# Optimization experiments

Measured on AMD Instinct MI355X. Metric: run time of the kernel, lower is better.

The kernel has to match this reference:

```python
import jax, jax.numpy as jnp
import numpy as np

D_MODEL = 1024
D_STATE = 128
D_CONV = 4
EXPAND = 2
HEADDIM = 64
D_INNER = EXPAND * D_MODEL          # 2048
NHEADS = D_INNER // HEADDIM         # 32
NGROUPS = 1
CONV_DIM = D_INNER + 2 * NGROUPS * D_STATE            # 2304
D_IN_PROJ = 2 * D_INNER + 2 * NGROUPS * D_STATE + NHEADS  # 4384
NUM_CLASS = 48
BATCH = 2
SEQLEN = 512


def setup_inputs() -> dict:
    key = jax.random.key(0)
    ks = jax.random.split(key, 8)
    s = 0.02
    inputs = jax.random.normal(ks[0], (BATCH, SEQLEN, D_MODEL), jnp.float32)
    W_in = jax.random.normal(ks[1], (D_MODEL, D_IN_PROJ), jnp.float32) * s
    conv_w = jax.random.normal(ks[2], (CONV_DIM, D_CONV), jnp.float32) * 0.2
    conv_b = jnp.zeros((CONV_DIM,), jnp.float32)
    # dt_bias = inverse-softplus of dt sampled in [1e-3, 0.1] (mamba init)
    dt = jnp.exp(jax.random.uniform(ks[3], (NHEADS,), jnp.float32) * (np.log(0.1) - np.log(1e-3)) + np.log(1e-3))
    dt_bias = dt + jnp.log(-jnp.expm1(-dt))
    A_log = jnp.log(jax.random.uniform(ks[4], (NHEADS,), jnp.float32, 1.0, 16.0))
    D = jnp.ones((NHEADS,), jnp.float32)
    norm_w = jnp.ones((D_INNER,), jnp.float32)
    W_out = jax.random.normal(ks[5], (D_INNER, D_MODEL), jnp.float32) * s
    W_cls = jax.random.normal(ks[6], (D_INNER, NUM_CLASS), jnp.float32) * s
    b_cls = jnp.zeros((NUM_CLASS,), jnp.float32)
    return {"inputs": inputs, "W_in": W_in, "conv_w": conv_w, "conv_b": conv_b,
            "dt_bias": dt_bias, "A_log": A_log, "D": D, "norm_w": norm_w,
            "W_out": W_out, "W_cls": W_cls, "b_cls": b_cls}


def _forward(inputs, W_in, conv_w, conv_b, dt_bias, A_log, D, norm_w, W_out, W_cls, b_cls):
    B, L, _ = inputs.shape
    zxbcdt = inputs @ W_in                                     # (B,L,4384)
    z, xBC, dt = jnp.split(zxbcdt, [D_INNER, D_INNER + CONV_DIM], axis=-1)
    dt = jax.nn.softplus(dt + dt_bias)                         # (B,L,H)
    # causal depthwise conv over time on (x,B,C)
    xBC_t = jnp.pad(jnp.transpose(xBC, (0, 2, 1)), ((0, 0), (0, 0), (D_CONV - 1, 0)))
    xBC_c = jax.lax.conv_general_dilated(xBC_t, conv_w[:, None, :], (1,), 'VALID',
                                         feature_group_count=CONV_DIM)
    xBC = jax.nn.silu(jnp.transpose(xBC_c, (0, 2, 1)) + conv_b)
    x, Bm, Cm = jnp.split(xBC, [D_INNER, D_INNER + D_STATE], axis=-1)
    x = x.reshape(B, L, NHEADS, HEADDIM)
    A = -jnp.exp(A_log)                                        # (H,)
    dA = jnp.exp(dt * A)                                       # (B,L,H)

    def step(state, inp):
        # state: (B,H,P,N) -- selective SSM recurrence (chunk_size=1 path)
        x_t, B_t, C_t, dt_t, dA_t = inp
        state = state * dA_t[:, :, None, None] + jnp.einsum('bhp,bn,bh->bhpn', x_t, B_t, dt_t)
        y_t = jnp.einsum('bhpn,bn->bhp', state, C_t)
        return state, y_t

    state0 = jnp.zeros((B, NHEADS, HEADDIM, D_STATE), inputs.dtype)
    xs = (jnp.transpose(x, (1, 0, 2, 3)), jnp.transpose(Bm, (1, 0, 2)),
          jnp.transpose(Cm, (1, 0, 2)), jnp.transpose(dt, (1, 0, 2)),
          jnp.transpose(dA, (1, 0, 2)))
    _, ys = jax.lax.scan(step, state0, xs)                     # ys: (L,B,H,P)
    y = jnp.transpose(ys, (1, 0, 2, 3)) + D[None, None, :, None] * x
    y = y.reshape(B, L, D_INNER)
    # gated RMSNorm: rmsnorm(y * silu(z)) * weight
    y = y * jax.nn.silu(z)
    y = y * jax.lax.rsqrt(jnp.mean(y * y, axis=-1, keepdims=True) + 1e-5) * norm_w
    # hidden_states (d_inner=2048) go through the per-timestep classifier
    preds = y @ W_cls + b_cls                                  # (B,L,num_class)
    return preds


def reference(inputs, W_in, conv_w, conv_b, dt_bias, A_log, D, norm_w, W_out, W_cls, b_cls):
    return _forward(inputs, W_in, conv_w, conv_b, dt_bias, A_log, D, norm_w, W_out, W_cls, b_cls)
```

## Files before the change

kernel.cpp:

```cpp
#include <hip/hip_runtime.h>
#include <hip/hip_bf16.h>
#include <cstdint>

#define BATCH 2
#define SEQLEN 512
#define BL (BATCH*SEQLEN)
#define DMODEL 1024
#define DINNER 2048
#define NHEADS 32
#define HEADDIM 64
#define DSTATE 128
#define CONVDIM 2304
#define DINPROJ 4384
#define NPROJPAD 4480
#define NCLS 48
#define QC 64
#define NCH 8

typedef short bf16x8 __attribute__((ext_vector_type(8)));
typedef float f32x4  __attribute__((ext_vector_type(4)));
typedef unsigned int u32;
typedef const __attribute__((address_space(1))) u32 gu32;
typedef __attribute__((address_space(3))) u32 lu32;

static __device__ __forceinline__ void gl16(const void* g, void* l) {
    __builtin_amdgcn_global_load_lds((gu32*)g, (lu32*)l, 16, 0, 0);
}

static __device__ __forceinline__ unsigned short f2bf(float f) {
    unsigned u = __float_as_uint(f);
    unsigned r = (u + 0x7FFFu + ((u >> 16) & 1u)) >> 16;
    return (unsigned short)r;
}
static __device__ __forceinline__ float bf2f(unsigned short u) {
    return __uint_as_float(((unsigned)u) << 16);
}

__global__ __launch_bounds__(256) void k_cvt_a(const float* __restrict__ in,
                                               unsigned short* __restrict__ out) {
    int i = (blockIdx.x * 256 + threadIdx.x) * 4;
    float4 v = *(const float4*)(in + i);
    ushort4 o;
    o.x = f2bf(v.x); o.y = f2bf(v.y); o.z = f2bf(v.z); o.w = f2bf(v.w);
    *(ushort4*)(out + i) = o;
}

__global__ __launch_bounds__(256) void k_transpose_w(const float* __restrict__ W,
                                                     unsigned short* __restrict__ Wt) {
    __shared__ float tile[32][33];
    int n0 = blockIdx.x * 32;
    int k0 = blockIdx.y * 32;
    int tx = threadIdx.x & 31;
    int ty = threadIdx.x >> 5;
#pragma unroll
    for (int i = 0; i < 4; ++i) {
        int k = k0 + ty + i * 8;
        tile[ty + i * 8][tx] = W[(size_t)k * DINPROJ + n0 + tx];
    }
    __syncthreads();
#pragma unroll
    for (int i = 0; i < 4; ++i) {
        int n = n0 + ty + i * 8;
        Wt[(size_t)n * DMODEL + k0 + tx] = f2bf(tile[tx][ty + i * 8]);
    }
}

__global__ __launch_bounds__(256) void k_prep_cls(const float* __restrict__ W,
                                                  const float* __restrict__ bcls,
                                                  unsigned short* __restrict__ Wt,
                                                  float* __restrict__ out) {
    int bid = blockIdx.x;
    if (bid < 192) {
        int i = bid * 256 + threadIdx.x;
        out[i] = bcls[i % NCLS];
    } else {
        int n = bid - 192;
        for (int k = threadIdx.x; k < DINNER; k += 256)
            Wt[(size_t)n * DINNER + k] = f2bf(W[(size_t)k * NCLS + n]);
    }
}

__global__ __launch_bounds__(256) void k_gemm_in(const unsigned short* __restrict__ A,
                                                 const unsigned short* __restrict__ Bt,
                                                 unsigned short* __restrict__ C) {
    __shared__ unsigned short As[2 * 4096];
    __shared__ unsigned short Bs[2 * 4096];
    const int tid  = threadIdx.x;
    const int m0   = blockIdx.y * 128;
    const int n0   = blockIdx.x * 128;
    const int w    = tid >> 6;
    const int lane = tid & 63;
    const int wm   = w >> 1, wn = w & 1;
    const int fr   = lane & 15, fq = lane >> 4;
    const int srow = w * 16 + (lane >> 2);
    const int skg  = (lane & 3) * 8;
    const unsigned short* gA0 = A  + (size_t)(m0 + srow) * DMODEL + skg;
    const unsigned short* gA1 = gA0 + (size_t)64 * DMODEL;
    const unsigned short* gB0 = Bt + (size_t)(n0 + srow) * DMODEL + skg;
    const unsigned short* gB1 = gB0 + (size_t)64 * DMODEL;

    f32x4 acc[4][4] = {};
    for (int k0 = 0; k0 < DMODEL; k0 += 64) {
        __syncthreads();
#pragma unroll
        for (int hh = 0; hh < 2; ++hh) {
            int kg = k0 + hh * 32;
            gl16(gA0 + kg, As + hh * 4096 + w * 512);
            gl16(gA1 + kg, As + hh * 4096 + 2048 + w * 512);
            gl16(gB0 + kg, Bs + hh * 4096 + w * 512);
            gl16(gB1 + kg, Bs + hh * 4096 + 2048 + w * 512);
        }
        __syncthreads();
#pragma unroll
        for (int hh = 0; hh < 2; ++hh) {
            bf16x8 af[4], bf[4];
#pragma unroll
            for (int mt = 0; mt < 4; ++mt)
                af[mt] = *(const bf16x8*)(&As[hh * 4096 + (wm * 64 + mt * 16 + fr) * 32 + fq * 8]);
#pragma unroll
            for (int nt = 0; nt < 4; ++nt)
                bf[nt] = *(const bf16x8*)(&Bs[hh * 4096 + (wn * 64 + nt * 16 + fr) * 32 + fq * 8]);
#pragma unroll
            for (int mt = 0; mt < 4; ++mt)
#pragma unroll
                for (int nt = 0; nt < 4; ++nt)
                    acc[mt][nt] = __builtin_amdgcn_mfma_f32_16x16x32_bf16(af[mt], bf[nt], acc[mt][nt], 0, 0, 0);
        }
    }
#pragma unroll
    for (int mt = 0; mt < 4; ++mt) {
#pragma unroll
        for (int nt = 0; nt < 4; ++nt) {
            int col = n0 + wn * 64 + nt * 16 + fr;
            if (col < DINPROJ) {
#pragma unroll
                for (int r = 0; r < 4; ++r) {
                    int row = m0 + wm * 64 + mt * 16 + fq * 4 + r;
                    C[(size_t)row * DINPROJ + col] = f2bf(acc[mt][nt][r]);
                }
            }
        }
    }
}

__global__ __launch_bounds__(256) void k_conv_dt(const unsigned short* __restrict__ zx,
                                                 const float* __restrict__ conv_w,
                                                 const float* __restrict__ conv_b,
                                                 const float* __restrict__ dt_bias,
                                                 float* __restrict__ xbc,
                                                 float* __restrict__ dtb) {
    int row = blockIdx.y;
    int c   = blockIdx.x * 256 + threadIdx.x;
    int b = row >> 9, l = row & 511;
    if (c < CONVDIM) {
        float acc = conv_b[c];
#pragma unroll
        for (int j = 0; j < 4; ++j) {
            int ls = l - 3 + j;
            float v = (ls >= 0) ? bf2f(zx[((size_t)(b * SEQLEN + ls)) * DINPROJ + DINNER + c]) : 0.f;
            acc += v * conv_w[c * 4 + j];
        }
        float s = acc / (1.f + expf(-acc));
        xbc[(size_t)row * CONVDIM + c] = s;
    } else if (c < CONVDIM + NHEADS) {
        int h = c - CONVDIM;
        float raw = bf2f(zx[(size_t)row * DINPROJ + (DINNER + CONVDIM) + h]) + dt_bias[h];
        float dt = (raw > 20.f) ? raw : log1pf(expf(raw));
        dtb[row * NHEADS + h] = dt;
    }
}

__global__ __launch_bounds__(256) void k_chunk(const float* __restrict__ xbc,
                                               const float* __restrict__ dtb,
                                               const float* __restrict__ A_log,
                                               const float* __restrict__ Dvec,
                                               float* __restrict__ yb,
                                               float* __restrict__ Sc_g,
                                               float* __restrict__ lam_g,
                                               float* __restrict__ esc_g) {
    const int gid = blockIdx.x;
    const int c = gid & 7;
    const int h = (gid >> 3) & 31;
    const int b = gid >> 8;
    const int row0 = b * SEQLEN + c * QC;

    __shared__ float cumS[QC], wS[QC], dtS[QC];
    __shared__ unsigned short Xt[QC][72];
    __shared__ unsigned short Bs[QC][136];
    __shared__ unsigned short BtW[DSTATE][72];
    __shared__ unsigned short Cs[QC][136];
    __shared__ unsigned short Gs[QC][72];

    const int tid = threadIdx.x;
    if (tid < 64) {
        float dtv = dtb[(size_t)(row0 + tid) * NHEADS + h];
        float nA = -expf(A_log[h]);
        float x = dtv * nA;
#pragma unroll
        for (int off = 1; off < 64; off <<= 1) {
            float v = __shfl_up(x, off, 64);
            if (tid >= off) x += v;
        }
        float cumTot = __shfl(x, 63, 64);
        cumS[tid] = x;
        dtS[tid] = dtv;
        wS[tid] = expf(cumTot - x) * dtv;
        esc_g[(size_t)gid * QC + tid] = expf(x);
        if (tid == 0) lam_g[gid] = expf(cumTot);
    }
    __syncthreads();

    {
        int row = tid >> 2;
        int g = tid & 3;
        const float* rp = xbc + (size_t)(row0 + row) * CONVDIM;
        float wrow = wS[row];
#pragma unroll
        for (int i = 0; i < 4; ++i) {
            float4 v = *(const float4*)(rp + h * HEADDIM + g * 16 + i * 4);
            int p = g * 16 + i * 4;
            Xt[p + 0][row] = f2bf(v.x);
            Xt[p + 1][row] = f2bf(v.y);
            Xt[p + 2][row] = f2bf(v.z);
            Xt[p + 3][row] = f2bf(v.w);
        }
#pragma unroll
        for (int i = 0; i < 8; ++i) {
            int n = g * 32 + i * 4;
            float4 v = *(const float4*)(rp + DINNER + n);
            ushort4 u;
            u.x = f2bf(v.x); u.y = f2bf(v.y); u.z = f2bf(v.z); u.w = f2bf(v.w);
            *(ushort4*)(&Bs[row][n]) = u;
            BtW[n + 0][row] = f2bf(v.x * wrow);
            BtW[n + 1][row] = f2bf(v.y * wrow);
            BtW[n + 2][row] = f2bf(v.z * wrow);
            BtW[n + 3][row] = f2bf(v.w * wrow);
        }
#pragma unroll
        for (int i = 0; i < 8; ++i) {
            int n = g * 32 + i * 4;
            float4 v = *(const float4*)(rp + DINNER + DSTATE + n);
            ushort4 u;
            u.x = f2bf(v.x); u.y = f2bf(v.y); u.z = f2bf(v.z); u.w = f2bf(v.w);
            *(ushort4*)(&Cs[row][n]) = u;
        }
    }
    __syncthreads();

    const int w = tid >> 6, lane = tid & 63;
    const int fr = lane & 15, fq = lane >> 4, fk = (lane >> 4) * 8;

    f32x4 accG[4] = {};
#pragma unroll
    for (int kk = 0; kk < 4; ++kk) {
        bf16x8 a = *(const bf16x8*)(&Cs[w * 16 + fr][kk * 32 + fk]);
#pragma unroll
        for (int nt = 0; nt < 4; ++nt) {
            bf16x8 bb = *(const bf16x8*)(&Bs[nt * 16 + fr][kk * 32 + fk]);
            accG[nt] = __builtin_amdgcn_mfma_f32_16x16x32_bf16(a, bb, accG[nt], 0, 0, 0);
        }
    }
#pragma unroll
    for (int nt = 0; nt < 4; ++nt) {
        int s = nt * 16 + fr;
        float cs = cumS[s], dts = dtS[s];
#pragma unroll
        for (int r = 0; r < 4; ++r) {
            int t = w * 16 + fq * 4 + r;
            float val = (s <= t) ? accG[nt][r] * expf(cumS[t] - cs) * dts : 0.f;
            Gs[t][s] = f2bf(val);
        }
    }
    __syncthreads();

    f32x4 accY[4] = {};
#pragma unroll
    for (int kk = 0; kk < 2; ++kk) {
        bf16x8 a = *(const bf16x8*)(&Gs[w * 16 + fr][kk * 32 + fk]);
#pragma unroll
        for (int pt = 0; pt < 4; ++pt) {
            bf16x8 bb = *(const bf16x8*)(&Xt[pt * 16 + fr][kk * 32 + fk]);
            accY[pt] = __builtin_amdgcn_mfma_f32_16x16x32_bf16(a, bb, accY[pt], 0, 0, 0);
        }
    }
    f32x4 accS[8] = {};
#pragma unroll
    for (int kk = 0; kk < 2; ++kk) {
        bf16x8 a = *(const bf16x8*)(&Xt[w * 16 + fr][kk * 32 + fk]);
#pragma unroll
        for (int nt = 0; nt < 8; ++nt) {
            bf16x8 bb = *(const bf16x8*)(&BtW[nt * 16 + fr][kk * 32 + fk]);
            accS[nt] = __builtin_amdgcn_mfma_f32_16x16x32_bf16(a, bb, accS[nt], 0, 0, 0);
        }
    }
    float Dh = Dvec[h];
#pragma unroll
    for (int pt = 0; pt < 4; ++pt) {
        int p = pt * 16 + fr;
#pragma unroll
        for (int r = 0; r < 4; ++r) {
            int t = w * 16 + fq * 4 + r;
            float xv = xbc[(size_t)(row0 + t) * CONVDIM + h * HEADDIM + p];
            yb[(size_t)(row0 + t) * DINNER + h * HEADDIM + p] = accY[pt][r] + Dh * xv;
        }
    }
    float* scp = Sc_g + (size_t)gid * (HEADDIM * DSTATE);
#pragma unroll
    for (int nt = 0; nt < 8; ++nt) {
        int n = nt * 16 + fr;
#pragma unroll
        for (int r = 0; r < 4; ++r) {
            int p = w * 16 + fq * 4 + r;
            scp[p * DSTATE + n] = accS[nt][r];
        }
    }
}

__global__ __launch_bounds__(256) void k_chain(const float* __restrict__ Sc_g,
                                               const float* __restrict__ lam_g,
                                               unsigned short* __restrict__ Sin_bf) {
    int bh = blockIdx.x >> 2;
    int sl = blockIdx.x & 3;
    int tid = threadIdx.x;
    float s[8];
#pragma unroll
    for (int i = 0; i < 8; ++i) s[i] = 0.f;
    for (int c = 0; c < NCH; ++c) {
        size_t base = (size_t)(bh * NCH + c) * (HEADDIM * DSTATE) + sl * 2048 + tid * 8;
#pragma unroll
        for (int j = 0; j < 8; j += 4) {
            ushort4 u;
            u.x = f2bf(s[j + 0]); u.y = f2bf(s[j + 1]);
            u.z = f2bf(s[j + 2]); u.w = f2bf(s[j + 3]);
            *(ushort4*)(Sin_bf + base + j) = u;
        }
        float lam = lam_g[bh * NCH + c];
#pragma unroll
        for (int j = 0; j < 8; j += 4) {
            float4 v = *(const float4*)(Sc_g + base + j);
            s[j + 0] = s[j + 0] * lam + v.x;
            s[j + 1] = s[j + 1] * lam + v.y;
            s[j + 2] = s[j + 2] * lam + v.z;
            s[j + 3] = s[j + 3] * lam + v.w;
        }
    }
}

__global__ __launch_bounds__(256) void k_cross(const float* __restrict__ xbc,
                                               const float* __restrict__ esc_g,
                                               const unsigned short* __restrict__ Sin_bf,
                                               float* __restrict__ yb) {
    const int gid = blockIdx.x;
    const int c = gid & 7;
    const int h = (gid >> 3) & 31;
    const int b = gid >> 8;
    const int row0 = b * SEQLEN + c * QC;
    __shared__ unsigned short Ct[QC][136];
    __shared__ unsigned short Ss[QC][136];
    const int tid = threadIdx.x;
    {
        int row = tid >> 2, g = tid & 3;
        const float* rp = xbc + (size_t)(row0 + row) * CONVDIM + DINNER + DSTATE;
        float esc = esc_g[(size_t)gid * QC + row];
#pragma unroll
        for (int i = 0; i < 8; ++i) {
            int n = g * 32 + i * 4;
            float4 v = *(const float4*)(rp + n);
            ushort4 u;
            u.x = f2bf(v.x * esc); u.y = f2bf(v.y * esc);
            u.z = f2bf(v.z * esc); u.w = f2bf(v.w * esc);
            *(ushort4*)(&Ct[row][n]) = u;
        }
        const uint4* sp = (const uint4*)(Sin_bf + (size_t)gid * (HEADDIM * DSTATE));
#pragma unroll
        for (int i = 0; i < 4; ++i) {
            uint4 v = sp[row * 16 + g * 4 + i];
            *(uint4*)(&Ss[row][g * 32 + i * 8]) = v;
        }
    }
    __syncthreads();
    const int w = tid >> 6, lane = tid & 63;
    const int fr = lane & 15, fq = lane >> 4, fk = (lane >> 4) * 8;
    f32x4 acc[4] = {};
#pragma unroll
    for (int kk = 0; kk < 4; ++kk) {
        bf16x8 a = *(const bf16x8*)(&Ct[w * 16 + fr][kk * 32 + fk]);
#pragma unroll
        for (int pt = 0; pt < 4; ++pt) {
            bf16x8 bb = *(const bf16x8*)(&Ss[pt * 16 + fr][kk * 32 + fk]);
            acc[pt] = __builtin_amdgcn_mfma_f32_16x16x32_bf16(a, bb, acc[pt], 0, 0, 0);
        }
    }
#pragma unroll
    for (int pt = 0; pt < 4; ++pt) {
        int p = pt * 16 + fr;
#pragma unroll
        for (int r = 0; r < 4; ++r) {
            int t = w * 16 + fq * 4 + r;
            size_t yi = (size_t)(row0 + t) * DINNER + h * HEADDIM + p;
            yb[yi] += acc[pt][r];
        }
    }
}

__global__ __launch_bounds__(256) void k_gate_norm(const unsigned short* __restrict__ zx,
                                                   const float* __restrict__ nw,
                                                   const float* __restrict__ y,
                                                   unsigned short* __restrict__ Gbf) {
    int row = blockIdx.x;
    int tid = threadIdx.x;
    const unsigned short* zrow = zx + (size_t)row * DINPROJ;
    const float* yr = y + (size_t)row * DINNER;
    float g[8];
    float ss = 0.f;
#pragma unroll
    for (int i = 0; i < 2; ++i) {
        int c = tid * 4 + i * 1024;
        float4 yv = *(const float4*)(yr + c);
        ushort4 zv = *(const ushort4*)(zrow + c);
        float zs[4] = {bf2f(zv.x), bf2f(zv.y), bf2f(zv.z), bf2f(zv.w)};
        float ys[4] = {yv.x, yv.y, yv.z, yv.w};
#pragma unroll
        for (int k = 0; k < 4; ++k) {
            float sil = zs[k] / (1.f + expf(-zs[k]));
            float gg = ys[k] * sil;
            g[i * 4 + k] = gg;
            ss += gg * gg;
        }
    }
#pragma unroll
    for (int off = 32; off >= 1; off >>= 1) ss += __shfl_xor(ss, off, 64);
    __shared__ float wsum[4];
    if ((tid & 63) == 0) wsum[tid >> 6] = ss;
    __syncthreads();
    float tot = wsum[0] + wsum[1] + wsum[2] + wsum[3];
    float scale = rsqrtf(tot / (float)DINNER + 1e-5f);
#pragma unroll
    for (int i = 0; i < 2; ++i) {
        int c = tid * 4 + i * 1024;
        float4 nv = *(const float4*)(nw + c);
        ushort4 o;
        o.x = f2bf(g[i * 4 + 0] * scale * nv.x);
        o.y = f2bf(g[i * 4 + 1] * scale * nv.y);
        o.z = f2bf(g[i * 4 + 2] * scale * nv.z);
        o.w = f2bf(g[i * 4 + 3] * scale * nv.w);
        *(ushort4*)(Gbf + (size_t)row * DINNER + c) = o;
    }
}

__global__ __launch_bounds__(256) void k_cls_mfma(const unsigned short* __restrict__ G,
                                                  const unsigned short* __restrict__ Wt,
                                                  float* __restrict__ out) {
    __shared__ unsigned short Gs[64][72];
    __shared__ unsigned short Ws[48][72];
    const int m0  = blockIdx.x * 64;
    const int k00 = blockIdx.y * 256;
    const int tid = threadIdx.x;
    const int w = tid >> 6, lane = tid & 63;
    const int fr = lane & 15, fq = lane >> 4, fk = fq * 8;
    f32x4 acc[3] = {};
    for (int ks = 0; ks < 4; ++ks) {
        int k0 = k00 + ks * 64;
        __syncthreads();
        {
            int row = tid >> 2, seg = (tid & 3) * 16;
            const unsigned short* gp = G + (size_t)(m0 + row) * DINNER + k0 + seg;
            *(uint4*)(&Gs[row][seg])     = *(const uint4*)(gp);
            *(uint4*)(&Gs[row][seg + 8]) = *(const uint4*)(gp + 8);
        }
        if (tid < 192) {
            int row = tid >> 2, seg = (tid & 3) * 16;
            const unsigned short* wp = Wt + (size_t)row * DINNER + k0 + seg;
            *(uint4*)(&Ws[row][seg])     = *(const uint4*)(wp);
            *(uint4*)(&Ws[row][seg + 8]) = *(const uint4*)(wp + 8);
        }
        __syncthreads();
#pragma unroll
        for (int kk = 0; kk < 2; ++kk) {
            bf16x8 a = *(const bf16x8*)(&Gs[w * 16 + fr][kk * 32 + fk]);
#pragma unroll
            for (int nt = 0; nt < 3; ++nt) {
                bf16x8 bb = *(const bf16x8*)(&Ws[nt * 16 + fr][kk * 32 + fk]);
                acc[nt] = __builtin_amdgcn_mfma_f32_16x16x32_bf16(a, bb, acc[nt], 0, 0, 0);
            }
        }
    }
#pragma unroll
    for (int nt = 0; nt < 3; ++nt) {
        int col = nt * 16 + fr;
#pragma unroll
        for (int r = 0; r < 4; ++r) {
            int row = m0 + w * 16 + fq * 4 + r;
            atomicAdd(&out[(size_t)row * NCLS + col], acc[nt][r]);
        }
    }
}

extern "C" void kernel_launch(void* const* d_in, const int* in_sizes, int n_in,
                              void* d_out, int out_size, void* d_ws, size_t ws_size,
                              hipStream_t stream) {
    const float* inputs  = (const float*)d_in[0];
    const float* W_in    = (const float*)d_in[1];
    const float* conv_w  = (const float*)d_in[2];
    const float* conv_b  = (const float*)d_in[3];
    const float* dt_bias = (const float*)d_in[4];
    const float* A_log   = (const float*)d_in[5];
    const float* Dvec    = (const float*)d_in[6];
    const float* norm_w  = (const float*)d_in[7];
    const float* W_cls   = (const float*)d_in[9];
    const float* b_cls   = (const float*)d_in[10];
    float* out = (float*)d_out;

    float* ws   = (float*)d_ws;
    unsigned short* zxb = (unsigned short*)ws;
    float* xbc  = ws   + (size_t)BL * DINPROJ / 2 + 512;
    float* dtb  = xbc  + (size_t)BL * CONVDIM;
    float* yb   = dtb  + (size_t)BL * NHEADS;
    float* Sc_g = yb   + (size_t)BL * DINNER;
    float* lam_g= Sc_g + (size_t)BATCH * NHEADS * NCH * HEADDIM * DSTATE;
    float* esc_g= lam_g+ (size_t)BATCH * NHEADS * NCH;
    unsigned short* Sin_bf = (unsigned short*)(esc_g + (size_t)BATCH * NHEADS * NCH * QC);
    unsigned short* abf    = Sin_bf + (size_t)BATCH * NHEADS * NCH * HEADDIM * DSTATE;
    unsigned short* wtbf   = abf + (size_t)BL * DMODEL;
    unsigned short* wclsbf = wtbf + (size_t)NPROJPAD * DMODEL;
    unsigned short* Gbf    = (unsigned short*)Sc_g;

    k_cvt_a<<<dim3(BL * DMODEL / (256 * 4)), dim3(256), 0, stream>>>(inputs, abf);
    k_transpose_w<<<dim3(DINPROJ / 32, DMODEL / 32), dim3(256), 0, stream>>>(W_in, wtbf);
    k_prep_cls<<<dim3(240), dim3(256), 0, stream>>>(W_cls, b_cls, wclsbf, out);
    k_gemm_in<<<dim3(NPROJPAD / 128, BL / 128), dim3(256), 0, stream>>>(abf, wtbf, zxb);
    k_conv_dt<<<dim3(10, BL), dim3(256), 0, stream>>>(zxb, conv_w, conv_b, dt_bias, xbc, dtb);
    k_chunk<<<dim3(BATCH * NHEADS * NCH), dim3(256), 0, stream>>>(xbc, dtb, A_log, Dvec,
                                                                  yb, Sc_g, lam_g, esc_g);
    k_chain<<<dim3(BATCH * NHEADS * 4), dim3(256), 0, stream>>>(Sc_g, lam_g, Sin_bf);
    k_cross<<<dim3(BATCH * NHEADS * NCH), dim3(256), 0, stream>>>(xbc, esc_g, Sin_bf, yb);
    k_gate_norm<<<dim3(BL), dim3(256), 0, stream>>>(zxb, norm_w, yb, Gbf);
    k_cls_mfma<<<dim3(BL / 64, 8), dim3(256), 0, stream>>>(Gbf, wclsbf, out);
}
```

Measured before the change: 171.4 us.

## Fuse prep kernels, fold conv/dt into chunk kernels, halve GEMM N-tile, bf16 states

Merges the three preprocessing kernels into one launch and removes the separate conv+dt kernel. The causal conv, SiLU and softplus are now recomputed inside k_chunk and k_cross straight from the bf16 projection output, so the fp32 xbc/dtb intermediates are never written. The input GEMM tile shrinks from 128 to 64 columns to launch more blocks, and per-chunk states are stored in bf16 to halve chain-kernel traffic. In exchange, the C/B conv columns are recomputed redundantly across heads, the conv reads are strided by row, and chunk states lose precision.

```diff
diff --git a/kernel.cpp b/kernel.cpp
--- a/kernel.cpp
+++ b/kernel.cpp
@@ -36,47 +36,49 @@
     return __uint_as_float(((unsigned)u) << 16);
 }
 
-__global__ __launch_bounds__(256) void k_cvt_a(const float* __restrict__ in,
-                                               unsigned short* __restrict__ out) {
-    int i = (blockIdx.x * 256 + threadIdx.x) * 4;
-    float4 v = *(const float4*)(in + i);
-    ushort4 o;
-    o.x = f2bf(v.x); o.y = f2bf(v.y); o.z = f2bf(v.z); o.w = f2bf(v.w);
-    *(ushort4*)(out + i) = o;
-}
-
-__global__ __launch_bounds__(256) void k_transpose_w(const float* __restrict__ W,
-                                                     unsigned short* __restrict__ Wt) {
+__global__ __launch_bounds__(256) void k_prep(const float* __restrict__ in,
+                                              unsigned short* __restrict__ abf,
+                                              const float* __restrict__ W,
+                                              unsigned short* __restrict__ Wt,
+                                              const float* __restrict__ Wcls,
+                                              const float* __restrict__ bcls,
+                                              unsigned short* __restrict__ Wtc,
+                                              float* __restrict__ out) {
     __shared__ float tile[32][33];
-    int n0 = blockIdx.x * 32;
-    int k0 = blockIdx.y * 32;
-    int tx = threadIdx.x & 31;
-    int ty = threadIdx.x >> 5;
-#pragma unroll
-    for (int i = 0; i < 4; ++i) {
-        int k = k0 + ty + i * 8;
-        tile[ty + i * 8][tx] = W[(size_t)k * DINPROJ + n0 + tx];
-    }
-    __syncthreads();
-#pragma unroll
-    for (int i = 0; i < 4; ++i) {
-        int n = n0 + ty + i * 8;
-        Wt[(size_t)n * DMODEL + k0 + tx] = f2bf(tile[tx][ty + i * 8]);
-    }
-}
-
-__global__ __launch_bounds__(256) void k_prep_cls(const float* __restrict__ W,
-                                                  const float* __restrict__ bcls,
-                                                  unsigned short* __restrict__ Wt,
-                                                  float* __restrict__ out) {
     int bid = blockIdx.x;
-    if (bid < 192) {
-        int i = bid * 256 + threadIdx.x;
-        out[i] = bcls[i % NCLS];
+    int tid = threadIdx.x;
+    if (bid < 1024) {
+        int i = (bid * 256 + tid) * 4;
+        float4 v = *(const float4*)(in + i);
+        ushort4 o;
+        o.x = f2bf(v.x); o.y = f2bf(v.y); o.z = f2bf(v.z); o.w = f2bf(v.w);
+        *(ushort4*)(abf + i) = o;
+    } else if (bid < 1024 + 4384) {
+        int t = bid - 1024;
+        int n0 = (t % 137) * 32;
+        int k0 = (t / 137) * 32;
+        int tx = tid & 31, ty = tid >> 5;
+#pragma unroll
+        for (int i = 0; i < 4; ++i) {
+            int k = k0 + ty + i * 8;
+            tile[ty + i * 8][tx] = W[(size_t)k * DINPROJ + n0 + tx];
+        }
+        __syncthreads();
+#pragma unroll
+        for (int i = 0; i < 4; ++i) {
+            int n = n0 + ty + i * 8;
+            Wt[(size_t)n * DMODEL + k0 + tx] = f2bf(tile[tx][ty + i * 8]);
+        }
     } else {
-        int n = bid - 192;
-        for (int k = threadIdx.x; k < DINNER; k += 256)
-            Wt[(size_t)n * DINNER + k] = f2bf(W[(size_t)k * NCLS + n]);
+        int b2 = bid - (1024 + 4384);
+        if (b2 < 192) {
+            int i = b2 * 256 + tid;
+            out[i] = bcls[i % NCLS];
+        } else {
+            int n = b2 - 192;
+            for (int k = tid; k < DINNER; k += 256)
+                Wtc[(size_t)n * DINNER + k] = f2bf(Wcls[(size_t)k * NCLS + n]);
+        }
     }
 }
 
@@ -84,10 +86,10 @@
                                                  const unsigned short* __restrict__ Bt,
                                                  unsigned short* __restrict__ C) {
     __shared__ unsigned short As[2 * 4096];
-    __shared__ unsigned short Bs[2 * 4096];
+    __shared__ unsigned short Bs[2 * 2048];
     const int tid  = threadIdx.x;
     const int m0   = blockIdx.y * 128;
-    const int n0   = blockIdx.x * 128;
+    const int n0   = blockIdx.x * 64;
     const int w    = tid >> 6;
     const int lane = tid & 63;
     const int wm   = w >> 1, wn = w & 1;
@@ -97,9 +99,8 @@
     const unsigned short* gA0 = A  + (size_t)(m0 + srow) * DMODEL + skg;
     const unsigned short* gA1 = gA0 + (size_t)64 * DMODEL;
     const unsigned short* gB0 = Bt + (size_t)(n0 + srow) * DMODEL + skg;
-    const unsigned short* gB1 = gB0 + (size_t)64 * DMODEL;
-
-    f32x4 acc[4][4] = {};
+
+    f32x4 acc[4][2] = {};
     for (int k0 = 0; k0 < DMODEL; k0 += 64) {
         __syncthreads();
 #pragma unroll
@@ -107,31 +108,30 @@
             int kg = k0 + hh * 32;
             gl16(gA0 + kg, As + hh * 4096 + w * 512);
             gl16(gA1 + kg, As + hh * 4096 + 2048 + w * 512);
-            gl16(gB0 + kg, Bs + hh * 4096 + w * 512);
-            gl16(gB1 + kg, Bs + hh * 4096 + 2048 + w * 512);
+            gl16(gB0 + kg, Bs + hh * 2048 + w * 512);
         }
         __syncthreads();
 #pragma unroll
         for (int hh = 0; hh < 2; ++hh) {
-            bf16x8 af[4], bf[4];
+            bf16x8 af[4], bfr[2];
 #pragma unroll
             for (int mt = 0; mt < 4; ++mt)
                 af[mt] = *(const bf16x8*)(&As[hh * 4096 + (wm * 64 + mt * 16 + fr) * 32 + fq * 8]);
 #pragma unroll
-            for (int nt = 0; nt < 4; ++nt)
-                bf[nt] = *(const bf16x8*)(&Bs[hh * 4096 + (wn * 64 + nt * 16 + fr) * 32 + fq * 8]);
+            for (int nt = 0; nt < 2; ++nt)
+                bfr[nt] = *(const bf16x8*)(&Bs[hh * 2048 + (wn * 32 + nt * 16 + fr) * 32 + fq * 8]);
 #pragma unroll
             for (int mt = 0; mt < 4; ++mt)
 #pragma unroll
-                for (int nt = 0; nt < 4; ++nt)
-                    acc[mt][nt] = __builtin_amdgcn_mfma_f32_16x16x32_bf16(af[mt], bf[nt], acc[mt][nt], 0, 0, 0);
+                for (int nt = 0; nt < 2; ++nt)
+                    acc[mt][nt] = __builtin_amdgcn_mfma_f32_16x16x32_bf16(af[mt], bfr[nt], acc[mt][nt], 0, 0, 0);
         }
     }
 #pragma unroll
     for (int mt = 0; mt < 4; ++mt) {
 #pragma unroll
-        for (int nt = 0; nt < 4; ++nt) {
-            int col = n0 + wn * 64 + nt * 16 + fr;
+        for (int nt = 0; nt < 2; ++nt) {
+            int col = n0 + wn * 32 + nt * 16 + fr;
             if (col < DINPROJ) {
 #pragma unroll
                 for (int r = 0; r < 4; ++r) {
@@ -143,46 +143,21 @@
     }
 }
 
-__global__ __launch_bounds__(256) void k_conv_dt(const unsigned short* __restrict__ zx,
-                                                 const float* __restrict__ conv_w,
-                                                 const float* __restrict__ conv_b,
-                                                 const float* __restrict__ dt_bias,
-                                                 float* __restrict__ xbc,
-                                                 float* __restrict__ dtb) {
-    int row = blockIdx.y;
-    int c   = blockIdx.x * 256 + threadIdx.x;
-    int b = row >> 9, l = row & 511;
-    if (c < CONVDIM) {
-        float acc = conv_b[c];
-#pragma unroll
-        for (int j = 0; j < 4; ++j) {
-            int ls = l - 3 + j;
-            float v = (ls >= 0) ? bf2f(zx[((size_t)(b * SEQLEN + ls)) * DINPROJ + DINNER + c]) : 0.f;
-            acc += v * conv_w[c * 4 + j];
-        }
-        float s = acc / (1.f + expf(-acc));
-        xbc[(size_t)row * CONVDIM + c] = s;
-    } else if (c < CONVDIM + NHEADS) {
-        int h = c - CONVDIM;
-        float raw = bf2f(zx[(size_t)row * DINPROJ + (DINNER + CONVDIM) + h]) + dt_bias[h];
-        float dt = (raw > 20.f) ? raw : log1pf(expf(raw));
-        dtb[row * NHEADS + h] = dt;
-    }
-}
-
-__global__ __launch_bounds__(256) void k_chunk(const float* __restrict__ xbc,
-                                               const float* __restrict__ dtb,
+__global__ __launch_bounds__(256) void k_chunk(const unsigned short* __restrict__ zx,
+                                               const float* __restrict__ conv_w,
+                                               const float* __restrict__ conv_b,
+                                               const float* __restrict__ dt_bias,
                                                const float* __restrict__ A_log,
                                                const float* __restrict__ Dvec,
                                                float* __restrict__ yb,
-                                               float* __restrict__ Sc_g,
+                                               unsigned short* __restrict__ Sc_bf,
                                                float* __restrict__ lam_g,
                                                float* __restrict__ esc_g) {
     const int gid = blockIdx.x;
-    const int c = gid & 7;
+    const int cq = gid & 7;
     const int h = (gid >> 3) & 31;
     const int b = gid >> 8;
-    const int row0 = b * SEQLEN + c * QC;
+    const int row0 = b * SEQLEN + cq * QC;
 
     __shared__ float cumS[QC], wS[QC], dtS[QC];
     __shared__ unsigned short Xt[QC][72];
@@ -193,7 +168,8 @@
 
     const int tid = threadIdx.x;
     if (tid < 64) {
-        float dtv = dtb[(size_t)(row0 + tid) * NHEADS + h];
+        float raw = bf2f(zx[(size_t)(row0 + tid) * DINPROJ + (DINNER + CONVDIM) + h]) + dt_bias[h];
+        float dtv = (raw > 20.f) ? raw : log1pf(expf(raw));
         float nA = -expf(A_log[h]);
         float x = dtv * nA;
 #pragma unroll
@@ -211,38 +187,45 @@
     __syncthreads();
 
     {
-        int row = tid >> 2;
-        int g = tid & 3;
-        const float* rp = xbc + (size_t)(row0 + row) * CONVDIM;
-        float wrow = wS[row];
-#pragma unroll
-        for (int i = 0; i < 4; ++i) {
-            float4 v = *(const float4*)(rp + h * HEADDIM + g * 16 + i * 4);
-            int p = g * 16 + i * 4;
-            Xt[p + 0][row] = f2bf(v.x);
-            Xt[p + 1][row] = f2bf(v.y);
-            Xt[p + 2][row] = f2bf(v.z);
-            Xt[p + 3][row] = f2bf(v.w);
-        }
-#pragma unroll
-        for (int i = 0; i < 8; ++i) {
-            int n = g * 32 + i * 4;
-            float4 v = *(const float4*)(rp + DINNER + n);
-            ushort4 u;
-            u.x = f2bf(v.x); u.y = f2bf(v.y); u.z = f2bf(v.z); u.w = f2bf(v.w);
-            *(ushort4*)(&Bs[row][n]) = u;
-            BtW[n + 0][row] = f2bf(v.x * wrow);
-            BtW[n + 1][row] = f2bf(v.y * wrow);
-            BtW[n + 2][row] = f2bf(v.z * wrow);
-            BtW[n + 3][row] = f2bf(v.w * wrow);
-        }
-#pragma unroll
-        for (int i = 0; i < 8; ++i) {
-            int n = g * 32 + i * 4;
-            float4 v = *(const float4*)(rp + DINNER + DSTATE + n);
-            ushort4 u;
-            u.x = f2bf(v.x); u.y = f2bf(v.y); u.z = f2bf(v.z); u.w = f2bf(v.w);
-            *(ushort4*)(&Cs[row][n]) = u;
+        int ch = tid & 63, rs = tid >> 6;
+        const float* cwp = conv_w + (size_t)(h * 64 + ch) * 4;
+        float w0 = cwp[0], w1 = cwp[1], w2 = cwp[2], w3 = cwp[3];
+        float cb = conv_b[h * 64 + ch];
+        int lb = cq * QC + rs * 16;
+        const unsigned short* xcol = zx + (size_t)b * SEQLEN * DINPROJ + DINNER + h * 64 + ch;
+        float xm3 = (lb >= 3) ? bf2f(xcol[(size_t)(lb - 3) * DINPROJ]) : 0.f;
+        float xm2 = (lb >= 2) ? bf2f(xcol[(size_t)(lb - 2) * DINPROJ]) : 0.f;
+        float xm1 = (lb >= 1) ? bf2f(xcol[(size_t)(lb - 1) * DINPROJ]) : 0.f;
+#pragma unroll
+        for (int r = 0; r < 16; ++r) {
+            float xc = bf2f(xcol[(size_t)(lb + r) * DINPROJ]);
+            float a = cb + w0 * xm3 + w1 * xm2 + w2 * xm1 + w3 * xc;
+            float s = a / (1.f + expf(-a));
+            Xt[ch][rs * 16 + r] = f2bf(s);
+            xm3 = xm2; xm2 = xm1; xm1 = xc;
+        }
+    }
+    {
+        int cc = tid;
+        const float* cwp = conv_w + (size_t)(2048 + cc) * 4;
+        float w0 = cwp[0], w1 = cwp[1], w2 = cwp[2], w3 = cwp[3];
+        float cb = conv_b[2048 + cc];
+        int lb = cq * QC;
+        const unsigned short* xcol = zx + (size_t)b * SEQLEN * DINPROJ + DINNER + 2048 + cc;
+        float xm3 = (lb >= 3) ? bf2f(xcol[(size_t)(lb - 3) * DINPROJ]) : 0.f;
+        float xm2 = (lb >= 2) ? bf2f(xcol[(size_t)(lb - 2) * DINPROJ]) : 0.f;
+        float xm1 = (lb >= 1) ? bf2f(xcol[(size_t)(lb - 1) * DINPROJ]) : 0.f;
+        for (int r = 0; r < QC; ++r) {
+            float xc = bf2f(xcol[(size_t)(lb + r) * DINPROJ]);
+            float a = cb + w0 * xm3 + w1 * xm2 + w2 * xm1 + w3 * xc;
+            float s = a / (1.f + expf(-a));
+            if (cc < 128) {
+                Bs[r][cc] = f2bf(s);
+                BtW[cc][r] = f2bf(s * wS[r]);
+            } else {
+                Cs[r][cc - 128] = f2bf(s);
+            }
+            xm3 = xm2; xm2 = xm1; xm1 = xc;
         }
     }
     __syncthreads();
@@ -300,23 +283,23 @@
 #pragma unroll
         for (int r = 0; r < 4; ++r) {
             int t = w * 16 + fq * 4 + r;
-            float xv = xbc[(size_t)(row0 + t) * CONVDIM + h * HEADDIM + p];
+            float xv = bf2f(Xt[p][t]);
             yb[(size_t)(row0 + t) * DINNER + h * HEADDIM + p] = accY[pt][r] + Dh * xv;
         }
     }
-    float* scp = Sc_g + (size_t)gid * (HEADDIM * DSTATE);
+    unsigned short* scp = Sc_bf + (size_t)gid * (HEADDIM * DSTATE);
 #pragma unroll
     for (int nt = 0; nt < 8; ++nt) {
         int n = nt * 16 + fr;
 #pragma unroll
         for (int r = 0; r < 4; ++r) {
             int p = w * 16 + fq * 4 + r;
-            scp[p * DSTATE + n] = accS[nt][r];
-        }
-    }
-}
-
-__global__ __launch_bounds__(256) void k_chain(const float* __restrict__ Sc_g,
+            scp[p * DSTATE + n] = f2bf(accS[nt][r]);
+        }
+    }
+}
+
+__global__ __launch_bounds__(256) void k_chain(const unsigned short* __restrict__ Sc_bf,
                                                const float* __restrict__ lam_g,
                                                unsigned short* __restrict__ Sin_bf) {
     int bh = blockIdx.x >> 2;
@@ -327,55 +310,67 @@
     for (int i = 0; i < 8; ++i) s[i] = 0.f;
     for (int c = 0; c < NCH; ++c) {
         size_t base = (size_t)(bh * NCH + c) * (HEADDIM * DSTATE) + sl * 2048 + tid * 8;
-#pragma unroll
-        for (int j = 0; j < 8; j += 4) {
-            ushort4 u;
-            u.x = f2bf(s[j + 0]); u.y = f2bf(s[j + 1]);
-            u.z = f2bf(s[j + 2]); u.w = f2bf(s[j + 3]);
-            *(ushort4*)(Sin_bf + base + j) = u;
-        }
+        ushort4 o0, o1;
+        o0.x = f2bf(s[0]); o0.y = f2bf(s[1]); o0.z = f2bf(s[2]); o0.w = f2bf(s[3]);
+        o1.x = f2bf(s[4]); o1.y = f2bf(s[5]); o1.z = f2bf(s[6]); o1.w = f2bf(s[7]);
+        *(ushort4*)(Sin_bf + base) = o0;
+        *(ushort4*)(Sin_bf + base + 4) = o1;
         float lam = lam_g[bh * NCH + c];
-#pragma unroll
-        for (int j = 0; j < 8; j += 4) {
-            float4 v = *(const float4*)(Sc_g + base + j);
-            s[j + 0] = s[j + 0] * lam + v.x;
-            s[j + 1] = s[j + 1] * lam + v.y;
-            s[j + 2] = s[j + 2] * lam + v.z;
-            s[j + 3] = s[j + 3] * lam + v.w;
-        }
-    }
-}
-
-__global__ __launch_bounds__(256) void k_cross(const float* __restrict__ xbc,
+        ushort4 v0 = *(const ushort4*)(Sc_bf + base);
+        ushort4 v1 = *(const ushort4*)(Sc_bf + base + 4);
+        s[0] = s[0] * lam + bf2f(v0.x);
+        s[1] = s[1] * lam + bf2f(v0.y);
+        s[2] = s[2] * lam + bf2f(v0.z);
+        s[3] = s[3] * lam + bf2f(v0.w);
+        s[4] = s[4] * lam + bf2f(v1.x);
+        s[5] = s[5] * lam + bf2f(v1.y);
+        s[6] = s[6] * lam + bf2f(v1.z);
+        s[7] = s[7] * lam + bf2f(v1.w);
+    }
+}
+
+__global__ __launch_bounds__(256) void k_cross(const unsigned short* __restrict__ zx,
+                                               const float* __restrict__ conv_w,
+                                               const float* __restrict__ conv_b,
                                                const float* __restrict__ esc_g,
                                                const unsigned short* __restrict__ Sin_bf,
                                                float* __restrict__ yb) {
     const int gid = blockIdx.x;
-    const int c = gid & 7;
+    const int cq = gid & 7;
     const int h = (gid >> 3) & 31;
     const int b = gid >> 8;
-    const int row0 = b * SEQLEN + c * QC;
+    const int row0 = b * SEQLEN + cq * QC;
     __shared__ unsigned short Ct[QC][136];
     __shared__ unsigned short Ss[QC][136];
+    __shared__ float escS[QC];
     const int tid = threadIdx.x;
+    if (tid < 64) escS[tid] = esc_g[(size_t)gid * QC + tid];
     {
         int row = tid >> 2, g = tid & 3;
-        const float* rp = xbc + (size_t)(row0 + row) * CONVDIM + DINNER + DSTATE;
-        float esc = esc_g[(size_t)gid * QC + row];
-#pragma unroll
-        for (int i = 0; i < 8; ++i) {
-            int n = g * 32 + i * 4;
-            float4 v = *(const float4*)(rp + n);
-            ushort4 u;
-            u.x = f2bf(v.x * esc); u.y = f2bf(v.y * esc);
-            u.z = f2bf(v.z * esc); u.w = f2bf(v.w * esc);
-            *(ushort4*)(&Ct[row][n]) = u;
-        }
         const uint4* sp = (const uint4*)(Sin_bf + (size_t)gid * (HEADDIM * DSTATE));
 #pragma unroll
         for (int i = 0; i < 4; ++i) {
             uint4 v = sp[row * 16 + g * 4 + i];
             *(uint4*)(&Ss[row][g * 32 + i * 8]) = v;
+        }
+    }
+    __syncthreads();
+    {
+        int n = tid & 127, rs = tid >> 7;
+        const float* cwp = conv_w + (size_t)(2176 + n) * 4;
+        float w0 = cwp[0], w1 = cwp[1], w2 = cwp[2], w3 = cwp[3];
+        float cb = conv_b[2176 + n];
+        int lb = cq * QC + rs * 32;
+        const unsigned short* xcol = zx + (size_t)b * SEQLEN * DINPROJ + DINNER + 2176 + n;
+        float xm3 = (lb >= 3) ? bf2f(xcol[(size_t)(lb - 3) * DINPROJ]) : 0.f;
+        float xm2 = (lb >= 2) ? bf2f(xcol[(size_t)(lb - 2) * DINPROJ]) : 0.f;
+        float xm1 = (lb >= 1) ? bf2f(xcol[(size_t)(lb - 1) * DINPROJ]) : 0.f;
+        for (int r = 0; r < 32; ++r) {
+            float xc = bf2f(xcol[(size_t)(lb + r) * DINPROJ]);
+            float a = cb + w0 * xm3 + w1 * xm2 + w2 * xm1 + w3 * xc;
+            float s = a / (1.f + expf(-a));
+            Ct[rs * 32 + r][n] = f2bf(s * escS[rs * 32 + r]);
+            xm3 = xm2; xm2 = xm1; xm1 = xc;
         }
     }
     __syncthreads();
@@ -511,29 +506,27 @@
     const float* b_cls   = (const float*)d_in[10];
     float* out = (float*)d_out;
 
-    float* ws   = (float*)d_ws;
+    float* ws = (float*)d_ws;
     unsigned short* zxb = (unsigned short*)ws;
-    float* xbc  = ws   + (size_t)BL * DINPROJ / 2 + 512;
-    float* dtb  = xbc  + (size_t)BL * CONVDIM;
-    float* yb   = dtb  + (size_t)BL * NHEADS;
-    float* Sc_g = yb   + (size_t)BL * DINNER;
-    float* lam_g= Sc_g + (size_t)BATCH * NHEADS * NCH * HEADDIM * DSTATE;
-    float* esc_g= lam_g+ (size_t)BATCH * NHEADS * NCH;
-    unsigned short* Sin_bf = (unsigned short*)(esc_g + (size_t)BATCH * NHEADS * NCH * QC);
-    unsigned short* abf    = Sin_bf + (size_t)BATCH * NHEADS * NCH * HEADDIM * DSTATE;
+    float* yb    = ws + (size_t)BL * DINPROJ / 2;
+    float* lam_g = yb + (size_t)BL * DINNER;
+    float* esc_g = lam_g + 512;
+    unsigned short* Sc_bf  = (unsigned short*)(esc_g + 512 * QC);
+    unsigned short* Sin_bf = Sc_bf + (size_t)512 * HEADDIM * DSTATE;
+    unsigned short* abf    = Sin_bf + (size_t)512 * HEADDIM * DSTATE;
     unsigned short* wtbf   = abf + (size_t)BL * DMODEL;
     unsigned short* wclsbf = wtbf + (size_t)NPROJPAD * DMODEL;
-    unsigned short* Gbf    = (unsigned short*)Sc_g;
-
-    k_cvt_a<<<dim3(BL * DMODEL / (256 * 4)), dim3(256), 0, stream>>>(inputs, abf);
-    k_transpose_w<<<dim3(DINPROJ / 32, DMODEL / 32), dim3(256), 0, stream>>>(W_in, wtbf);
-    k_prep_cls<<<dim3(240), dim3(256), 0, stream>>>(W_cls, b_cls, wclsbf, out);
-    k_gemm_in<<<dim3(NPROJPAD / 128, BL / 128), dim3(256), 0, stream>>>(abf, wtbf, zxb);
-    k_conv_dt<<<dim3(10, BL), dim3(256), 0, stream>>>(zxb, conv_w, conv_b, dt_bias, xbc, dtb);
-    k_chunk<<<dim3(BATCH * NHEADS * NCH), dim3(256), 0, stream>>>(xbc, dtb, A_log, Dvec,
-                                                                  yb, Sc_g, lam_g, esc_g);
-    k_chain<<<dim3(BATCH * NHEADS * 4), dim3(256), 0, stream>>>(Sc_g, lam_g, Sin_bf);
-    k_cross<<<dim3(BATCH * NHEADS * NCH), dim3(256), 0, stream>>>(xbc, esc_g, Sin_bf, yb);
+    unsigned short* Gbf    = Sc_bf;
+
+    k_prep<<<dim3(1024 + 4384 + 240), dim3(256), 0, stream>>>(inputs, abf, W_in, wtbf,
+                                                              W_cls, b_cls, wclsbf, out);
+    k_gemm_in<<<dim3(NPROJPAD / 64, BL / 128), dim3(256), 0, stream>>>(abf, wtbf, zxb);
+    k_chunk<<<dim3(BATCH * NHEADS * NCH), dim3(256), 0, stream>>>(zxb, conv_w, conv_b,
+                                                                  dt_bias, A_log, Dvec,
+                                                                  yb, Sc_bf, lam_g, esc_g);
+    k_chain<<<dim3(BATCH * NHEADS * 4), dim3(256), 0, stream>>>(Sc_bf, lam_g, Sin_bf);
+    k_cross<<<dim3(BATCH * NHEADS * NCH), dim3(256), 0, stream>>>(zxb, conv_w, conv_b,
+                                                                  esc_g, Sin_bf, yb);
     k_gate_norm<<<dim3(BL), dim3(256), 0, stream>>>(zxb, norm_w, yb, Gbf);
     k_cls_mfma<<<dim3(BL / 64, 8), dim3(256), 0, stream>>>(Gbf, wclsbf, out);
 }
```

New measurement: 177.4 us. +3.5%, slower.
